# Kernel tuning notes

Measured on AMD Instinct MI355X. Metric: run time of the kernel, lower is better.

Reference implementation:

```python
import jax, jax.numpy as jnp
import numpy as np

N, D = 8192, 128

def _rbf_kernel(x, y):
    # InfoVAE-style kernel: exp(-mean((x_i - y_j)^2) / dim) = exp(-sqdist / dim^2)
    dim = x.shape[1]
    x2 = jnp.sum(x * x, axis=1)              # [n]
    y2 = jnp.sum(y * y, axis=1)              # [m]
    sqdist = x2[:, None] + y2[None, :] - 2.0 * (x @ y.T)  # [n, m]
    return jnp.exp(-sqdist / (dim * dim))


def setup_inputs() -> dict:
    key = jax.random.key(0)
    k1, k2 = jax.random.split(key)
    inputs = jax.random.normal(k1, (N, D), dtype=jnp.float32)
    true_samples = jax.random.normal(k2, (N, D), dtype=jnp.float32)
    return {"inputs": inputs, "true_samples": true_samples}


def reference(inputs, true_samples):
    x = true_samples  # samples from standard normal prior
    y = inputs
    k_xx = _rbf_kernel(x, x)
    k_yy = _rbf_kernel(y, y)
    k_xy = _rbf_kernel(x, y)
    mmd = jnp.mean(k_xx) + jnp.mean(k_yy) - 2.0 * jnp.mean(k_xy)
    return mmd
```

## Files before the change

### kernel.cpp

```cpp
#include <hip/hip_runtime.h>
#include <hip/hip_bf16.h>
#include <math.h>


#define NN 8192
#define DD 128
#define TZ 16384
#define TILES 64
#define NBLOCKS (TILES * (TILES + 1) / 2)

typedef __attribute__((ext_vector_type(8))) short bf16x8;
typedef __attribute__((ext_vector_type(4))) float f32x4;
typedef __attribute__((ext_vector_type(2))) float f32x2;

#if __has_builtin(__builtin_amdgcn_exp2f)
#define EXP2F __builtin_amdgcn_exp2f
#else
#define EXP2F exp2f
#endif

constexpr float LOG2E = 0x1.715476p+0f;
constexpr float S2 = LOG2E / 8192.0f;

constexpr size_t WS_NORM = 2048;
constexpr size_t WS_Z    = WS_NORM + (size_t)TZ * sizeof(float);

__device__ __forceinline__ void gload_lds16(const void* g, void* l) {
  __builtin_amdgcn_global_load_lds(
      (const __attribute__((address_space(1))) void*)g,
      (__attribute__((address_space(3))) void*)l, 16, 0, 0);
}

__global__ __launch_bounds__(256) void prep(
    const float* __restrict__ X, const float* __restrict__ Y,
    __hip_bfloat16* __restrict__ Z, float* __restrict__ normZ,
    double* __restrict__ sums) {
  if (blockIdx.x == 0) sums[threadIdx.x] = 0.0;

  const int row = blockIdx.x * 4 + (threadIdx.x >> 6);
  const int lane = threadIdx.x & 63;
  const float* __restrict__ src =
      (row < NN) ? (X + (size_t)row * DD) : (Y + (size_t)(row - NN) * DD);
  const float2 v = *reinterpret_cast<const float2*>(src + 2 * lane);

  float n = v.x * v.x + v.y * v.y;
  *reinterpret_cast<__hip_bfloat162*>(Z + (size_t)row * DD + 2 * lane) =
      __hip_bfloat162{__float2bfloat16(v.x), __float2bfloat16(v.y)};

#pragma unroll
  for (int o = 32; o > 0; o >>= 1) n += __shfl_down(n, o);
  if (lane == 0) normZ[row] = n * (-LOG2E / 16384.0f);
}

__device__ __forceinline__ int tri_start(int i) {
  return i * TILES - (i * (i - 1)) / 2;
}

__global__ __launch_bounds__(512, 2) void mmd_mfma(
    const __hip_bfloat16* __restrict__ Z, const float* __restrict__ normZ,
    double* __restrict__ sums) {
  __shared__ alignas(16) char lds[2 * 32768 + 256];

  const int t = blockIdx.x;
  int I = (int)((129.0 - sqrt(129.0 * 129.0 - 8.0 * (double)t)) * 0.5);
  if (I > 63) I = 63;
  if (I < 0) I = 0;
  while (I < 63 && tri_start(I + 1) <= t) ++I;
  while (I > 0 && tri_start(I) > t) --I;
  const int J = I + (t - tri_start(I));

  const int tid = threadIdx.x;
  const int lane = tid & 63, wave = tid >> 6;
  const int wr = wave >> 2, wc = wave & 3;
  const int lr = lane & 15, quad = lane >> 4;

  const char* Zb = (const char*)Z;
  const int rd0 = (wave << 5) + (lane >> 2);
  const int gch = (lane & 3) ^ ((lane >> 3) & 3);
  const char* srcA = Zb + ((size_t)(I * 256 + rd0)) * 256 + gch * 16;
  const char* srcB = Zb + ((size_t)(J * 256 + rd0)) * 256 + gch * 16;
  char* ldw = lds + wave * 2048;

#define STAGE(s, buf) do {                                               \
    gload_lds16(srcA + (s) * 64,        ldw + (buf) * 32768);            \
    gload_lds16(srcA + (s) * 64 + 4096, ldw + (buf) * 32768 + 1024);     \
    gload_lds16(srcB + (s) * 64,        ldw + (buf) * 32768 + 16384);    \
    gload_lds16(srcB + (s) * 64 + 4096, ldw + (buf) * 32768 + 17408);    \
  } while (0)

  const int csw = (quad ^ ((lr >> 1) & 3)) << 4;
  const char* aRd = lds + (wr * 128 + lr) * 64 + csw;
  const char* bRd = lds + 16384 + (wc * 64 + lr) * 64 + csw;

  bf16x8 a[8], b[4];
  f32x4 acc[8][4] = {};

#define LOADFRAGS(buf) do {                                              \
    _Pragma("unroll")                                                    \
    for (int i = 0; i < 8; ++i)                                          \
      a[i] = *reinterpret_cast<const bf16x8*>(aRd + (buf) * 32768 + i * 1024); \
    _Pragma("unroll")                                                    \
    for (int j = 0; j < 4; ++j)                                          \
      b[j] = *reinterpret_cast<const bf16x8*>(bRd + (buf) * 32768 + j * 1024); \
  } while (0)

#define MFMAS() do {                                                     \
    _Pragma("unroll")                                                    \
    for (int i = 0; i < 8; ++i)                                          \
      _Pragma("unroll")                                                  \
      for (int j = 0; j < 4; ++j)                                        \
        acc[i][j] = __builtin_amdgcn_mfma_f32_16x16x32_bf16(             \
            a[i], b[j], acc[i][j], 0, 0, 0);                             \
  } while (0)

  STAGE(0, 0);
  STAGE(1, 1);

  asm volatile("s_waitcnt vmcnt(4)\n\ts_barrier" ::: "memory");
  LOADFRAGS(0);
  asm volatile("s_waitcnt lgkmcnt(0)\n\ts_barrier" ::: "memory");
  __builtin_amdgcn_sched_barrier(0);
  STAGE(2, 0);
  __builtin_amdgcn_sched_barrier(0);
  MFMAS();

  asm volatile("s_waitcnt vmcnt(4)\n\ts_barrier" ::: "memory");
  LOADFRAGS(1);
  asm volatile("s_waitcnt lgkmcnt(0)\n\ts_barrier" ::: "memory");
  __builtin_amdgcn_sched_barrier(0);
  STAGE(3, 1);
  __builtin_amdgcn_sched_barrier(0);
  MFMAS();

  asm volatile("s_waitcnt vmcnt(4)\n\ts_barrier" ::: "memory");
  LOADFRAGS(0);
  asm volatile("s_waitcnt lgkmcnt(0)" ::: "memory");
  __builtin_amdgcn_sched_barrier(0);
  MFMAS();

  asm volatile("s_waitcnt vmcnt(0)\n\ts_barrier" ::: "memory");
  LOADFRAGS(1);
  asm volatile("s_waitcnt lgkmcnt(0)" ::: "memory");
  __builtin_amdgcn_sched_barrier(0);
  MFMAS();

#undef STAGE
#undef LOADFRAGS
#undef MFMAS

  const float* nzA = normZ + I * 256 + wr * 128;
  const float* nzB = normZ + J * 256 + wc * 64;
  f32x4 ar[8];
  float cb[4];
#pragma unroll
  for (int i = 0; i < 8; ++i)
    ar[i] = *reinterpret_cast<const f32x4*>(nzA + i * 16 + quad * 4);
#pragma unroll
  for (int j = 0; j < 4; ++j) cb[j] = nzB[j * 16 + lr];

  const f32x2 s2v = {S2, S2};
  f32x2 part01 = {0.f, 0.f}, part23 = {0.f, 0.f};
#pragma unroll
  for (int i = 0; i < 8; ++i) {
    const f32x2 ar01 = {ar[i].x, ar[i].y};
    const f32x2 ar23 = {ar[i].z, ar[i].w};
#pragma unroll
    for (int j = 0; j < 4; ++j) {
      const f32x2 rb2 = {cb[j], cb[j]};
      const f32x2 base01 = ar01 + rb2;
      const f32x2 base23 = ar23 + rb2;
      const f32x2 acc01 = {acc[i][j][0], acc[i][j][1]};
      const f32x2 acc23 = {acc[i][j][2], acc[i][j][3]};
      const f32x2 arg01 = __builtin_elementwise_fma(acc01, s2v, base01);
      const f32x2 arg23 = __builtin_elementwise_fma(acc23, s2v, base23);
      part01 += (f32x2){EXP2F(arg01.x), EXP2F(arg01.y)};
      part23 += (f32x2){EXP2F(arg23.x), EXP2F(arg23.y)};
    }
  }
  const f32x2 ps = part01 + part23;
  double local = (double)(ps.x + ps.y);
  double w = ((I < 32) == (J < 32)) ? 1.0 : -1.0;
  if (I != J) w += w;
  local *= w;

#pragma unroll
  for (int o = 32; o > 0; o >>= 1) local += __shfl_down(local, o);
  if (lane == 0)
    atomicAdd(&sums[((t & 31) << 3) | wave], local);
}

__global__ void finish(const double* __restrict__ s, float* __restrict__ out) {
  double v = s[threadIdx.x] + s[threadIdx.x + 64] + s[threadIdx.x + 128] +
             s[threadIdx.x + 192];
#pragma unroll
  for (int o = 32; o > 0; o >>= 1) v += __shfl_down(v, o);
  if (threadIdx.x == 0)
    out[0] = (float)(v * (1.0 / ((double)NN * (double)NN)));
}

extern "C" void kernel_launch(void* const* d_in, const int* in_sizes, int n_in,
                              void* d_out, int out_size, void* d_ws, size_t ws_size,
                              hipStream_t stream) {
  const float* y_inputs = (const float*)d_in[0];
  const float* x_true   = (const float*)d_in[1];
  float* out = (float*)d_out;

  char* ws = (char*)d_ws;
  double* sums = (double*)ws;
  float* normZ = (float*)(ws + WS_NORM);
  __hip_bfloat16* Z = (__hip_bfloat16*)(ws + WS_Z);

  prep<<<TZ / 4, 256, 0, stream>>>(x_true, y_inputs, Z, normZ, sums);
  mmd_mfma<<<NBLOCKS, 512, 0, stream>>>(Z, normZ, sums);
  finish<<<1, 64, 0, stream>>>(sums, out);
}
```

Baseline: 116.5 us.

## Store bf16 operands in pre-swizzled K-planes and use 16-wave blocks

The prep kernel now writes bf16 data into four K-slice planes already laid out in the swizzled LDS order. Each wave can then fill its LDS region with one contiguous 16-byte-per-lane global-to-LDS load per operand per stage, instead of strided gathers. The main kernel moves to 1024 threads (16 waves) with 64x64 per-wave subtiles, which halves accumulator registers per thread and adds waves to hide latency. In exchange it gives up two-blocks-per-CU occupancy and adds more barrier participants per block.

```diff
diff --git a/kernel.cpp b/kernel.cpp
--- a/kernel.cpp
+++ b/kernel.cpp
@@ -22,6 +22,8 @@
 constexpr float LOG2E = 0x1.715476p+0f;
 constexpr float S2 = LOG2E / 8192.0f;
 
+constexpr size_t PLANE = 1048576;
+
 constexpr size_t WS_NORM = 2048;
 constexpr size_t WS_Z    = WS_NORM + (size_t)TZ * sizeof(float);
 
@@ -33,7 +35,7 @@
 
 __global__ __launch_bounds__(256) void prep(
     const float* __restrict__ X, const float* __restrict__ Y,
-    __hip_bfloat16* __restrict__ Z, float* __restrict__ normZ,
+    char* __restrict__ Zs, float* __restrict__ normZ,
     double* __restrict__ sums) {
   if (blockIdx.x == 0) sums[threadIdx.x] = 0.0;
 
@@ -44,7 +46,13 @@
   const float2 v = *reinterpret_cast<const float2*>(src + 2 * lane);
 
   float n = v.x * v.x + v.y * v.y;
-  *reinterpret_cast<__hip_bfloat162*>(Z + (size_t)row * DD + 2 * lane) =
+
+  const int ks = lane >> 4;
+  const int quadc = (lane >> 2) & 3;
+  const int inner = (lane & 3) * 4;
+  char* dst = Zs + (size_t)ks * PLANE + (size_t)row * 64 +
+              ((quadc ^ ((row >> 1) & 3)) << 4) + inner;
+  *reinterpret_cast<__hip_bfloat162*>(dst) =
       __hip_bfloat162{__float2bfloat16(v.x), __float2bfloat16(v.y)};
 
 #pragma unroll
@@ -56,8 +64,8 @@
   return i * TILES - (i * (i - 1)) / 2;
 }
 
-__global__ __launch_bounds__(512, 2) void mmd_mfma(
-    const __hip_bfloat16* __restrict__ Z, const float* __restrict__ normZ,
+__global__ __launch_bounds__(1024, 1) void mmd_mfma(
+    const char* __restrict__ Zs, const float* __restrict__ normZ,
     double* __restrict__ sums) {
   __shared__ alignas(16) char lds[2 * 32768 + 256];
 
@@ -74,30 +82,26 @@
   const int wr = wave >> 2, wc = wave & 3;
   const int lr = lane & 15, quad = lane >> 4;
 
-  const char* Zb = (const char*)Z;
-  const int rd0 = (wave << 5) + (lane >> 2);
-  const int gch = (lane & 3) ^ ((lane >> 3) & 3);
-  const char* srcA = Zb + ((size_t)(I * 256 + rd0)) * 256 + gch * 16;
-  const char* srcB = Zb + ((size_t)(J * 256 + rd0)) * 256 + gch * 16;
-  char* ldw = lds + wave * 2048;
+  const char* srcA = Zs + (size_t)I * 16384 + wave * 1024 + (lane << 4);
+  const char* srcB = Zs + (size_t)J * 16384 + wave * 1024 + (lane << 4);
+  char* ldwA = lds + wave * 1024;
+  char* ldwB = lds + 16384 + wave * 1024;
 
 #define STAGE(s, buf) do {                                               \
-    gload_lds16(srcA + (s) * 64,        ldw + (buf) * 32768);            \
-    gload_lds16(srcA + (s) * 64 + 4096, ldw + (buf) * 32768 + 1024);     \
-    gload_lds16(srcB + (s) * 64,        ldw + (buf) * 32768 + 16384);    \
-    gload_lds16(srcB + (s) * 64 + 4096, ldw + (buf) * 32768 + 17408);    \
+    gload_lds16(srcA + (size_t)(s) * PLANE, ldwA + (buf) * 32768);       \
+    gload_lds16(srcB + (size_t)(s) * PLANE, ldwB + (buf) * 32768);       \
   } while (0)
 
   const int csw = (quad ^ ((lr >> 1) & 3)) << 4;
-  const char* aRd = lds + (wr * 128 + lr) * 64 + csw;
+  const char* aRd = lds + (wr * 64 + lr) * 64 + csw;
   const char* bRd = lds + 16384 + (wc * 64 + lr) * 64 + csw;
 
-  bf16x8 a[8], b[4];
-  f32x4 acc[8][4] = {};
+  bf16x8 a[4], b[4];
+  f32x4 acc[4][4] = {};
 
 #define LOADFRAGS(buf) do {                                              \
     _Pragma("unroll")                                                    \
-    for (int i = 0; i < 8; ++i)                                          \
+    for (int i = 0; i < 4; ++i)                                          \
       a[i] = *reinterpret_cast<const bf16x8*>(aRd + (buf) * 32768 + i * 1024); \
     _Pragma("unroll")                                                    \
     for (int j = 0; j < 4; ++j)                                          \
@@ -106,7 +110,7 @@
 
 #define MFMAS() do {                                                     \
     _Pragma("unroll")                                                    \
-    for (int i = 0; i < 8; ++i)                                          \
+    for (int i = 0; i < 4; ++i)                                          \
       _Pragma("unroll")                                                  \
       for (int j = 0; j < 4; ++j)                                        \
         acc[i][j] = __builtin_amdgcn_mfma_f32_16x16x32_bf16(             \
@@ -116,7 +120,7 @@
   STAGE(0, 0);
   STAGE(1, 1);
 
-  asm volatile("s_waitcnt vmcnt(4)\n\ts_barrier" ::: "memory");
+  asm volatile("s_waitcnt vmcnt(2)\n\ts_barrier" ::: "memory");
   LOADFRAGS(0);
   asm volatile("s_waitcnt lgkmcnt(0)\n\ts_barrier" ::: "memory");
   __builtin_amdgcn_sched_barrier(0);
@@ -124,7 +128,7 @@
   __builtin_amdgcn_sched_barrier(0);
   MFMAS();
 
-  asm volatile("s_waitcnt vmcnt(4)\n\ts_barrier" ::: "memory");
+  asm volatile("s_waitcnt vmcnt(2)\n\ts_barrier" ::: "memory");
   LOADFRAGS(1);
   asm volatile("s_waitcnt lgkmcnt(0)\n\ts_barrier" ::: "memory");
   __builtin_amdgcn_sched_barrier(0);
@@ -132,7 +136,7 @@
   __builtin_amdgcn_sched_barrier(0);
   MFMAS();
 
-  asm volatile("s_waitcnt vmcnt(4)\n\ts_barrier" ::: "memory");
+  asm volatile("s_waitcnt vmcnt(2)\n\ts_barrier" ::: "memory");
   LOADFRAGS(0);
   asm volatile("s_waitcnt lgkmcnt(0)" ::: "memory");
   __builtin_amdgcn_sched_barrier(0);
@@ -148,12 +152,12 @@
 #undef LOADFRAGS
 #undef MFMAS
 
-  const float* nzA = normZ + I * 256 + wr * 128;
+  const float* nzA = normZ + I * 256 + wr * 64;
   const float* nzB = normZ + J * 256 + wc * 64;
-  f32x4 ar[8];
+  f32x4 ar[4];
   float cb[4];
 #pragma unroll
-  for (int i = 0; i < 8; ++i)
+  for (int i = 0; i < 4; ++i)
     ar[i] = *reinterpret_cast<const f32x4*>(nzA + i * 16 + quad * 4);
 #pragma unroll
   for (int j = 0; j < 4; ++j) cb[j] = nzB[j * 16 + lr];
@@ -161,7 +165,7 @@
   const f32x2 s2v = {S2, S2};
   f32x2 part01 = {0.f, 0.f}, part23 = {0.f, 0.f};
 #pragma unroll
-  for (int i = 0; i < 8; ++i) {
+  for (int i = 0; i < 4; ++i) {
     const f32x2 ar01 = {ar[i].x, ar[i].y};
     const f32x2 ar23 = {ar[i].z, ar[i].w};
 #pragma unroll
@@ -186,7 +190,7 @@
 #pragma unroll
   for (int o = 32; o > 0; o >>= 1) local += __shfl_down(local, o);
   if (lane == 0)
-    atomicAdd(&sums[((t & 31) << 3) | wave], local);
+    atomicAdd(&sums[((t & 15) << 4) | wave], local);
 }
 
 __global__ void finish(const double* __restrict__ s, float* __restrict__ out) {
@@ -208,9 +212,9 @@
   char* ws = (char*)d_ws;
   double* sums = (double*)ws;
   float* normZ = (float*)(ws + WS_NORM);
-  __hip_bfloat16* Z = (__hip_bfloat16*)(ws + WS_Z);
-
-  prep<<<TZ / 4, 256, 0, stream>>>(x_true, y_inputs, Z, normZ, sums);
-  mmd_mfma<<<NBLOCKS, 512, 0, stream>>>(Z, normZ, sums);
+  char* Zs = ws + WS_Z;
+
+  prep<<<TZ / 4, 256, 0, stream>>>(x_true, y_inputs, Zs, normZ, sums);
+  mmd_mfma<<<NBLOCKS, 1024, 0, stream>>>(Zs, normZ, sums);
   finish<<<1, 64, 0, stream>>>(sums, out);
 }
```

After: 119.1 us. 2.2% more time.
